# Performance work log

Measured on AMD Instinct MI355X. Metric: run time of the kernel, lower is better.

Reference implementation:

```python
import jax, jax.numpy as jnp
import numpy as np

N = 100000
E = 1000000
IN_DIM = 64
OUT_DIM = 64


def setup_inputs() -> dict:
    key = jax.random.key(0)
    k1, k2, k3, k4 = jax.random.split(key, 4)
    x = jax.random.normal(k1, (N, IN_DIM), dtype=jnp.float32)
    edge_index = jax.random.randint(k2, (2, E), 0, N, dtype=jnp.int64)
    # nn.Linear(in_dim, out_dim): weight (out,in), bias (out,)
    bound = 1.0 / np.sqrt(IN_DIM)
    W = jax.random.uniform(k3, (OUT_DIM, IN_DIM), dtype=jnp.float32, minval=-bound, maxval=bound)
    b = jax.random.uniform(k4, (OUT_DIM,), dtype=jnp.float32, minval=-bound, maxval=bound)
    return {"x": x, "edge_index": edge_index, "W": W, "b": b}


def reference(x, edge_index, W, b):
    i = edge_index[0]  # target nodes (E,)
    j = edge_index[1]  # source nodes (E,)
    msg = x[j] @ W.T + b  # (E, out_dim)
    n = x.shape[0]
    out = jax.ops.segment_sum(msg, i, num_segments=n)  # (N, out_dim)
    deg = jax.ops.segment_sum(jnp.ones((i.shape[0],), dtype=msg.dtype), i, num_segments=n)
    deg = jnp.maximum(deg, 1.0)[:, None]
    return out / deg
```

## Files before the change

kernel.cpp:

```cpp
#include <hip/hip_runtime.h>

constexpr int N_NODES = 100000;
constexpr int N_EDGES = 1000000;
constexpr int DIM = 64;

constexpr int SCAN_BLK = 512;
constexpr int NBLK = (N_NODES + SCAN_BLK - 1) / SCAN_BLK;

__global__ __launch_bounds__(256) void count_ticket(
    const int* __restrict__ eidx, int* __restrict__ deg, int* __restrict__ ticket)
{
    int e = blockIdx.x * 256 + threadIdx.x;
    if (e >= N_EDGES) return;
    int i = eidx[e];
    ticket[e] = atomicAdd(&deg[i], 1);
}

__global__ __launch_bounds__(SCAN_BLK) void scan_block(
    const int* __restrict__ deg, int* __restrict__ offs, int* __restrict__ bsums)
{
    __shared__ int s[SCAN_BLK];
    int n = blockIdx.x * SCAN_BLK + threadIdx.x;
    int v = (n < N_NODES) ? deg[n] : 0;
    s[threadIdx.x] = v;
    __syncthreads();
    for (int d = 1; d < SCAN_BLK; d <<= 1) {
        int t = (threadIdx.x >= d) ? s[threadIdx.x - d] : 0;
        __syncthreads();
        s[threadIdx.x] += t;
        __syncthreads();
    }
    if (n < N_NODES) offs[n] = s[threadIdx.x] - v;
    if (threadIdx.x == SCAN_BLK - 1) bsums[blockIdx.x] = s[SCAN_BLK - 1];
}

__global__ __launch_bounds__(256) void scan_sums(int* __restrict__ bsums)
{
    __shared__ int s[256];
    int v = (threadIdx.x < NBLK) ? bsums[threadIdx.x] : 0;
    s[threadIdx.x] = v;
    __syncthreads();
    for (int d = 1; d < 256; d <<= 1) {
        int t = (threadIdx.x >= d) ? s[threadIdx.x - d] : 0;
        __syncthreads();
        s[threadIdx.x] += t;
        __syncthreads();
    }
    if (threadIdx.x < NBLK) bsums[threadIdx.x] = s[threadIdx.x] - v;
}

__global__ __launch_bounds__(SCAN_BLK) void add_base(
    int* __restrict__ offs, const int* __restrict__ bsums)
{
    int n = blockIdx.x * SCAN_BLK + threadIdx.x;
    if (n >= N_NODES) return;
    offs[n] += bsums[blockIdx.x];
}

__global__ __launch_bounds__(256) void scatter_kernel(
    const int* __restrict__ eidx, const int* __restrict__ offs,
    const int* __restrict__ ticket, int* __restrict__ bucket)
{
    int e = blockIdx.x * 256 + threadIdx.x;
    if (e >= N_EDGES) return;
    int i = eidx[e];
    int j = eidx[N_EDGES + e];
    bucket[offs[i] + ticket[e]] = j;
}

__global__ __launch_bounds__(256) void transform_kernel(
    const float* __restrict__ x, const float* __restrict__ W, float* __restrict__ y)
{
    int n = blockIdx.x * 256 + threadIdx.x;
    if (n >= N_NODES) return;

    float h[DIM];
    const float4* xrow = (const float4*)(x + (size_t)n * DIM);
#pragma unroll
    for (int k = 0; k < DIM / 4; ++k) {
        float4 v = xrow[k];
        h[4 * k + 0] = v.x; h[4 * k + 1] = v.y; h[4 * k + 2] = v.z; h[4 * k + 3] = v.w;
    }

    float4* yrow = (float4*)(y + (size_t)n * DIM);
#pragma unroll 1
    for (int d0 = 0; d0 < DIM; d0 += 4) {
        float a0 = 0.f, a1 = 0.f, a2 = 0.f, a3 = 0.f;
        const float* w0 = W + (size_t)(d0 + 0) * DIM;
        const float* w1 = W + (size_t)(d0 + 1) * DIM;
        const float* w2 = W + (size_t)(d0 + 2) * DIM;
        const float* w3 = W + (size_t)(d0 + 3) * DIM;
#pragma unroll
        for (int k = 0; k < DIM; ++k) {
            float hk = h[k];
            a0 = fmaf(hk, w0[k], a0);
            a1 = fmaf(hk, w1[k], a1);
            a2 = fmaf(hk, w2[k], a2);
            a3 = fmaf(hk, w3[k], a3);
        }
        float4 o; o.x = a0; o.y = a1; o.z = a2; o.w = a3;
        yrow[d0 / 4] = o;
    }
}

__global__ __launch_bounds__(256) void gather_kernel(
    const float* __restrict__ y, const int* __restrict__ offs,
    const int* __restrict__ deg, const int* __restrict__ bucket,
    const float* __restrict__ b, float* __restrict__ out)
{
    unsigned t = blockIdx.x * 256u + threadIdx.x;
    unsigned n = t >> 4;
    unsigned lane = t & 15u;
    if (n >= (unsigned)N_NODES) return;

    int start = offs[n];
    int d = deg[n];
    const float4* y4 = (const float4*)y;
    float4 acc = make_float4(0.f, 0.f, 0.f, 0.f);
    for (int e = 0; e < d; ++e) {
        int j = bucket[start + e];
        float4 v = y4[(size_t)j * (DIM / 4) + lane];
        acc.x += v.x; acc.y += v.y; acc.z += v.z; acc.w += v.w;
    }

    float4 o;
    if (d > 0) {
        float inv = 1.0f / (float)d;
        float4 bb = ((const float4*)b)[lane];
        o.x = acc.x * inv + bb.x;
        o.y = acc.y * inv + bb.y;
        o.z = acc.z * inv + bb.z;
        o.w = acc.w * inv + bb.w;
    } else {
        o = make_float4(0.f, 0.f, 0.f, 0.f);
    }
    ((float4*)out)[(size_t)n * (DIM / 4) + lane] = o;
}

extern "C" void kernel_launch(void* const* d_in, const int* in_sizes, int n_in,
                              void* d_out, int out_size, void* d_ws, size_t ws_size,
                              hipStream_t stream) {
    const float* x  = (const float*)d_in[0];
    const int*   ei = (const int*)d_in[1];
    const float* W  = (const float*)d_in[2];
    const float* b  = (const float*)d_in[3];
    float* out = (float*)d_out;

    float* y      = (float*)d_ws;
    int*   deg    = (int*)(y + (size_t)N_NODES * DIM);
    int*   offs   = deg + N_NODES;
    int*   ticket = offs + N_NODES;
    int*   bucket = ticket + N_EDGES;
    int*   bsums  = bucket + N_EDGES;

    hipMemsetAsync(deg, 0, N_NODES * sizeof(int), stream);

    count_ticket<<<(N_EDGES + 255) / 256, 256, 0, stream>>>(ei, deg, ticket);
    scan_block<<<NBLK, SCAN_BLK, 0, stream>>>(deg, offs, bsums);
    scan_sums<<<1, 256, 0, stream>>>(bsums);
    add_base<<<NBLK, SCAN_BLK, 0, stream>>>(offs, bsums);
    scatter_kernel<<<(N_EDGES + 255) / 256, 256, 0, stream>>>(ei, offs, ticket, bucket);
    transform_kernel<<<(N_NODES + 255) / 256, 256, 0, stream>>>(x, W, y);
    gather_kernel<<<(N_NODES * 16) / 256, 256, 0, stream>>>(y, offs, deg, bucket, b, out);
}
```

Before: 230.7 us.

## Fuse neighbor mean-aggregation with linear transform in one tiled kernel

Reorders the math so raw x rows are averaged per node first and then multiplied by W, instead of transforming every node and then gathering. The gather and the 64x64 matmul run in a single kernel that holds a 64-node tile in shared memory, which removes the intermediate y buffer and its write and read round trip. Each wave gathers full 64-float rows with 4-way unrolled independent loads, but the block-level syncs between the gather and matmul phases can limit latency hiding.

```diff
diff --git a/kernel.cpp b/kernel.cpp
--- a/kernel.cpp
+++ b/kernel.cpp
@@ -6,6 +6,9 @@
 
 constexpr int SCAN_BLK = 512;
 constexpr int NBLK = (N_NODES + SCAN_BLK - 1) / SCAN_BLK;
+
+constexpr int TILE = 64;
+constexpr int PAD = 65;
 
 __global__ __launch_bounds__(256) void count_ticket(
     const int* __restrict__ eidx, int* __restrict__ deg, int* __restrict__ ticket)
@@ -68,73 +71,82 @@
     bucket[offs[i] + ticket[e]] = j;
 }
 
-__global__ __launch_bounds__(256) void transform_kernel(
-    const float* __restrict__ x, const float* __restrict__ W, float* __restrict__ y)
+__global__ __launch_bounds__(256) void fused_gather_mm(
+    const float* __restrict__ x, const int* __restrict__ offs,
+    const int* __restrict__ deg, const int* __restrict__ bucket,
+    const float* __restrict__ W, const float* __restrict__ b,
+    float* __restrict__ out)
 {
-    int n = blockIdx.x * 256 + threadIdx.x;
-    if (n >= N_NODES) return;
+    __shared__ float tile[TILE * PAD];
 
-    float h[DIM];
-    const float4* xrow = (const float4*)(x + (size_t)n * DIM);
+    const int base = blockIdx.x * TILE;
+    const int lane = threadIdx.x & 63;
+    const int wid  = threadIdx.x >> 6;
+
+    for (int i = 0; i < 16; ++i) {
+        int row = wid * 16 + i;
+        int node = base + row;
+        float sum = 0.0f;
+        if (node < N_NODES) {
+            int start = __builtin_amdgcn_readfirstlane(offs[node]);
+            int d     = __builtin_amdgcn_readfirstlane(deg[node]);
+            int e = 0;
+            for (; e + 4 <= d; e += 4) {
+                int j0 = bucket[start + e + 0];
+                int j1 = bucket[start + e + 1];
+                int j2 = bucket[start + e + 2];
+                int j3 = bucket[start + e + 3];
+                float v0 = x[(size_t)j0 * DIM + lane];
+                float v1 = x[(size_t)j1 * DIM + lane];
+                float v2 = x[(size_t)j2 * DIM + lane];
+                float v3 = x[(size_t)j3 * DIM + lane];
+                sum += (v0 + v1) + (v2 + v3);
+            }
+            for (; e < d; ++e) {
+                int j = bucket[start + e];
+                sum += x[(size_t)j * DIM + lane];
+            }
+            float inv = (d > 0) ? 1.0f / (float)d : 0.0f;
+            sum *= inv;
+        }
+        tile[row * PAD + lane] = sum;
+    }
+    __syncthreads();
+
+    const int nd  = threadIdx.x & 63;
+    const int d0u = __builtin_amdgcn_readfirstlane((threadIdx.x >> 6) << 4);
+    const float* __restrict__ Wr = W + (size_t)d0u * DIM;
+
+    float acc[16];
 #pragma unroll
-    for (int k = 0; k < DIM / 4; ++k) {
-        float4 v = xrow[k];
-        h[4 * k + 0] = v.x; h[4 * k + 1] = v.y; h[4 * k + 2] = v.z; h[4 * k + 3] = v.w;
+    for (int q = 0; q < 16; ++q) acc[q] = 0.0f;
+
+#pragma unroll 4
+    for (int k = 0; k < DIM; ++k) {
+        float a = tile[nd * PAD + k];
+#pragma unroll
+        for (int q = 0; q < 16; ++q)
+            acc[q] = fmaf(a, Wr[(size_t)q * DIM + k], acc[q]);
     }
 
-    float4* yrow = (float4*)(y + (size_t)n * DIM);
-#pragma unroll 1
-    for (int d0 = 0; d0 < DIM; d0 += 4) {
-        float a0 = 0.f, a1 = 0.f, a2 = 0.f, a3 = 0.f;
-        const float* w0 = W + (size_t)(d0 + 0) * DIM;
-        const float* w1 = W + (size_t)(d0 + 1) * DIM;
-        const float* w2 = W + (size_t)(d0 + 2) * DIM;
-        const float* w3 = W + (size_t)(d0 + 3) * DIM;
+    int gnode = base + nd;
+    int dg = (gnode < N_NODES) ? deg[gnode] : 0;
+    __syncthreads();
 #pragma unroll
-        for (int k = 0; k < DIM; ++k) {
-            float hk = h[k];
-            a0 = fmaf(hk, w0[k], a0);
-            a1 = fmaf(hk, w1[k], a1);
-            a2 = fmaf(hk, w2[k], a2);
-            a3 = fmaf(hk, w3[k], a3);
-        }
-        float4 o; o.x = a0; o.y = a1; o.z = a2; o.w = a3;
-        yrow[d0 / 4] = o;
+    for (int q = 0; q < 16; ++q) {
+        float v = (dg > 0) ? (acc[q] + b[d0u + q]) : 0.0f;
+        tile[nd * PAD + d0u + q] = v;
     }
-}
+    __syncthreads();
 
-__global__ __launch_bounds__(256) void gather_kernel(
-    const float* __restrict__ y, const int* __restrict__ offs,
-    const int* __restrict__ deg, const int* __restrict__ bucket,
-    const float* __restrict__ b, float* __restrict__ out)
-{
-    unsigned t = blockIdx.x * 256u + threadIdx.x;
-    unsigned n = t >> 4;
-    unsigned lane = t & 15u;
-    if (n >= (unsigned)N_NODES) return;
-
-    int start = offs[n];
-    int d = deg[n];
-    const float4* y4 = (const float4*)y;
-    float4 acc = make_float4(0.f, 0.f, 0.f, 0.f);
-    for (int e = 0; e < d; ++e) {
-        int j = bucket[start + e];
-        float4 v = y4[(size_t)j * (DIM / 4) + lane];
-        acc.x += v.x; acc.y += v.y; acc.z += v.z; acc.w += v.w;
+#pragma unroll
+    for (int r = 0; r < 16; ++r) {
+        int idx = r * 256 + threadIdx.x;
+        int row = idx >> 6, d = idx & 63;
+        int g = base + row;
+        if (g < N_NODES)
+            out[(size_t)g * DIM + d] = tile[row * PAD + d];
     }
-
-    float4 o;
-    if (d > 0) {
-        float inv = 1.0f / (float)d;
-        float4 bb = ((const float4*)b)[lane];
-        o.x = acc.x * inv + bb.x;
-        o.y = acc.y * inv + bb.y;
-        o.z = acc.z * inv + bb.z;
-        o.w = acc.w * inv + bb.w;
-    } else {
-        o = make_float4(0.f, 0.f, 0.f, 0.f);
-    }
-    ((float4*)out)[(size_t)n * (DIM / 4) + lane] = o;
 }
 
 extern "C" void kernel_launch(void* const* d_in, const int* in_sizes, int n_in,
@@ -146,12 +158,11 @@
     const float* b  = (const float*)d_in[3];
     float* out = (float*)d_out;
 
-    float* y      = (float*)d_ws;
-    int*   deg    = (int*)(y + (size_t)N_NODES * DIM);
-    int*   offs   = deg + N_NODES;
-    int*   ticket = offs + N_NODES;
-    int*   bucket = ticket + N_EDGES;
-    int*   bsums  = bucket + N_EDGES;
+    int* deg    = (int*)d_ws;
+    int* offs   = deg + N_NODES;
+    int* ticket = offs + N_NODES;
+    int* bucket = ticket + N_EDGES;
+    int* bsums  = bucket + N_EDGES;
 
     hipMemsetAsync(deg, 0, N_NODES * sizeof(int), stream);
 
@@ -160,6 +171,6 @@
     scan_sums<<<1, 256, 0, stream>>>(bsums);
     add_base<<<NBLK, SCAN_BLK, 0, stream>>>(offs, bsums);
     scatter_kernel<<<(N_EDGES + 255) / 256, 256, 0, stream>>>(ei, offs, ticket, bucket);
-    transform_kernel<<<(N_NODES + 255) / 256, 256, 0, stream>>>(x, W, y);
-    gather_kernel<<<(N_NODES * 16) / 256, 256, 0, stream>>>(y, offs, deg, bucket, b, out);
+    fused_gather_mm<<<(N_NODES + TILE - 1) / TILE, 256, 0, stream>>>(
+        x, offs, deg, bucket, W, b, out);
 }
```

Result: faster. 198.1 us (-14.1%).
